# Kernel tuning notes

Hardware: AMD Instinct MI355X
Metric: run time of the kernel (lower is better)

Reference implementation:

```python
import jax, jax.numpy as jnp
import numpy as np

NM = 4096; NP = 4096; EM = 65536; EP = 65536; H = 256; HEADS = 4; G = 32


def _lin(k, din, dout):
    k1, k2 = jax.random.split(k)
    return (jax.random.normal(k1, (din, dout), jnp.float32) * (1.0 / np.sqrt(din)),
            jax.random.normal(k2, (dout,), jnp.float32) * 0.01)


def setup_inputs() -> dict:
    key = jax.random.key(0)
    ks = jax.random.split(key, 32)
    inp = {}
    inp['x_mol'] = jax.random.normal(ks[0], (NM, 8), jnp.float32)
    inp['x_prot'] = jax.random.normal(ks[1], (NP, 4), jnp.float32)
    inp['ea_mol'] = jax.random.normal(ks[2], (EM, 2), jnp.float32)
    inp['ea_prot'] = jax.random.normal(ks[3], (EP, 2), jnp.float32)
    inp['ei_mol'] = jax.random.randint(ks[4], (2, EM), 0, NM)
    inp['ei_prot'] = jax.random.randint(ks[5], (2, EP), 0, NP)
    inp['batch_mol'] = jnp.sort(jax.random.randint(ks[6], (NM,), 0, G))
    inp['batch_prot'] = jnp.sort(jax.random.randint(ks[7], (NP,), 0, G))
    inp['node_lin_mol_w'], inp['node_lin_mol_b'] = _lin(ks[8], 8, H)
    inp['node_lin_prot_w'], inp['node_lin_prot_b'] = _lin(ks[9], 4, H)
    inp['edge_lin_mol_w'], inp['edge_lin_mol_b'] = _lin(ks[10], 2, H)
    inp['edge_lin_prot_w'], inp['edge_lin_prot_b'] = _lin(ks[11], 2, H)
    # two GINE conv layers per graph, each with a 2-layer MLP; stack layer dim first
    for pref, base in (('mol', 12), ('prot', 16)):
        w1 = []; b1 = []; w2 = []; b2 = []
        for l in range(2):
            w, b = _lin(ks[base + 2 * l], H, H); w1.append(w); b1.append(b)
            w, b = _lin(ks[base + 2 * l + 1], H, H); w2.append(w); b2.append(b)
        inp[pref + '_w1'] = jnp.stack(w1); inp[pref + '_b1'] = jnp.stack(b1)
        inp[pref + '_w2'] = jnp.stack(w2); inp[pref + '_b2'] = jnp.stack(b2)
    for pref, base in (('mp', 20), ('pm', 23)):
        inp[pref + '_wq'], inp[pref + '_bq'] = _lin(ks[base], H, H)
        inp[pref + '_wk'], inp[pref + '_bk'] = _lin(ks[base + 1], H, H)
        inp[pref + '_wv'], inp[pref + '_bv'] = _lin(ks[base + 2], H, H)
    inp['fc1_w'], inp['fc1_b'] = _lin(ks[26], 2 * H, H)
    inp['fc2_w'], inp['fc2_b'] = _lin(ks[27], H, 1)
    return inp


def _gine_stack(x, ei, e, w1, b1, w2, b2):
    # GINEConv (eps=0): x_i' = relu(nn(x_i + sum_j relu(x_j + e_ji))), 2 layers, shared edge emb
    src, dst = ei[0], ei[1]
    n = x.shape[0]
    for l in range(w1.shape[0]):
        msg = jax.nn.relu(x[src] + e)                      # [E, H]
        agg = jax.ops.segment_sum(msg, dst, num_segments=n)  # [N, H]
        h = x + agg
        h = jax.nn.relu(h @ w1[l] + b1[l]) @ w2[l] + b2[l]
        x = jax.nn.relu(h)
    return x


def _cross_attn(qn, kn, wq, bq, wk, bk, wv, bv):
    nq, d = qn.shape
    nk = kn.shape[0]
    hd = d // HEADS
    Q = (qn @ wq + bq).reshape(nq, HEADS, hd)
    K = (kn @ wk + bk).reshape(nk, HEADS, hd)
    V = (kn @ wv + bv).reshape(nk, HEADS, hd)
    scores = jnp.einsum('qhd,khd->hqk', Q, K) / np.float32(hd ** 0.5)
    w = jax.nn.softmax(scores, axis=-1)
    return jnp.einsum('hqk,khd->qhd', w, V).reshape(nq, d)


def _seg_mean(h, seg, n):
    s = jax.ops.segment_sum(h, seg, num_segments=n)
    c = jax.ops.segment_sum(jnp.ones((h.shape[0], 1), h.dtype), seg, num_segments=n)
    return s / jnp.maximum(c, 1.0)


def reference(x_mol, x_prot, ea_mol, ea_prot, ei_mol, ei_prot, batch_mol, batch_prot,
              node_lin_mol_w, node_lin_mol_b, node_lin_prot_w, node_lin_prot_b,
              edge_lin_mol_w, edge_lin_mol_b, edge_lin_prot_w, edge_lin_prot_b,
              mol_w1, mol_b1, mol_w2, mol_b2, prot_w1, prot_b1, prot_w2, prot_b2,
              mp_wq, mp_bq, mp_wk, mp_bk, mp_wv, mp_bv,
              pm_wq, pm_bq, pm_wk, pm_bk, pm_wv, pm_bv,
              fc1_w, fc1_b, fc2_w, fc2_b):
    hm = x_mol @ node_lin_mol_w + node_lin_mol_b
    hp = x_prot @ node_lin_prot_w + node_lin_prot_b
    em = ea_mol @ edge_lin_mol_w + edge_lin_mol_b
    ep = ea_prot @ edge_lin_prot_w + edge_lin_prot_b
    H_mol = _gine_stack(hm, ei_mol, em, mol_w1, mol_b1, mol_w2, mol_b2)
    H_prot = _gine_stack(hp, ei_prot, ep, prot_w1, prot_b1, prot_w2, prot_b2)
    H_mol_c = H_mol + _cross_attn(H_mol, H_prot, mp_wq, mp_bq, mp_wk, mp_bk, mp_wv, mp_bv)
    H_prot_c = H_prot + _cross_attn(H_prot, H_mol, pm_wq, pm_bq, pm_wk, pm_bk, pm_wv, pm_bv)
    z_mol = _seg_mean(H_mol_c, batch_mol, G)
    z_prot = _seg_mean(H_prot_c, batch_prot, G)
    z = jnp.concatenate([z_mol, z_prot], axis=1)
    x = jax.nn.relu(z @ fc1_w + fc1_b)
    out = jax.nn.sigmoid(x @ fc2_w + fc2_b)
    return out.squeeze(-1)
```

## Files before the change

### kernel.cpp

```cpp
#include <hip/hip_runtime.h>
#include <math.h>

#define HDIM 256
#define NMOL 4096
#define NPROT 4096
#define NEDGE 65536
#define NG 32

typedef _Float16 f16x8 __attribute__((ext_vector_type(8)));
typedef _Float16 f16x4 __attribute__((ext_vector_type(4)));
typedef __attribute__((ext_vector_type(4))) float f32x4;

__device__ __forceinline__ void splitf(float x, _Float16& h, _Float16& l) {
  h = (_Float16)x;
  l = (_Float16)(x - (float)h);
}

struct __align__(16) EdgeRec { int src; float a0; float a1; int pad; };

struct PtrPack { const float* p[14]; };

__global__ __launch_bounds__(256) void k_prep_wt(PtrPack pk, _Float16* __restrict__ dh,
                                                 _Float16* __restrict__ dl) {
  __shared__ float Ts[64][68];
  const int m = blockIdx.z;
  const int n0 = blockIdx.y * 64, k0 = blockIdx.x * 64;
  const float* W = pk.p[m];
  const int t = threadIdx.x;
#pragma unroll
  for (int rep = 0; rep < 16; ++rep) {
    int k = rep * 4 + (t >> 6);
    int n = t & 63;
    Ts[n][k] = W[(size_t)(k0 + k) * 256 + n0 + n];
  }
  __syncthreads();
#pragma unroll
  for (int rep = 0; rep < 2; ++rep) {
    int idx = t + rep * 256;
    int nr = idx >> 3, koff = (idx & 7) * 8;
    f16x8 vh, vl;
#pragma unroll
    for (int i = 0; i < 8; ++i) {
      _Float16 h, l;
      splitf(Ts[nr][koff + i], h, l);
      vh[i] = h; vl[i] = l;
    }
    size_t off = (size_t)m * 65536 + (size_t)(n0 + nr) * 256 + k0 + koff;
    *(f16x8*)&dh[off] = vh;
    *(f16x8*)&dl[off] = vl;
  }
}

struct EmbJob {
  const float* x; const float* w; const float* b;
  _Float16* oh; _Float16* ol; int K;
};

__global__ __launch_bounds__(256) void k_node_embed2(EmbJob j0, EmbJob j1) {
  const EmbJob& j = blockIdx.y ? j1 : j0;
  const int i = blockIdx.x;
  const int c = threadIdx.x;
  float acc = j.b[c];
  for (int k = 0; k < j.K; ++k) acc += j.x[i * j.K + k] * j.w[k * HDIM + c];
  _Float16 h, l;
  splitf(acc, h, l);
  j.oh[(size_t)i * HDIM + c] = h;
  j.ol[(size_t)i * HDIM + c] = l;
}

__global__ __launch_bounds__(256) void k_csr_count2(const int* __restrict__ ei0,
                                                    const int* __restrict__ ei1,
                                                    int* __restrict__ cur0,
                                                    int* __restrict__ cur1, int E) {
  const int* ei = blockIdx.y ? ei1 : ei0;
  int* cur = blockIdx.y ? cur1 : cur0;
  const int e = blockIdx.x * 256 + threadIdx.x;
  if (e < E) atomicAdd(&cur[ei[E + e]], 1);
}

__global__ __launch_bounds__(256) void k_csr_scan2(int* __restrict__ c0, int* __restrict__ o0,
                                                   int* __restrict__ c1, int* __restrict__ o1,
                                                   int N) {
  int* cnt_cur = blockIdx.x ? c1 : c0;
  int* off = blockIdx.x ? o1 : o0;
  __shared__ int tsum[256], tpre[257];
  const int t = threadIdx.x;
  const int base = t * 16;
  int loc[16], s = 0;
#pragma unroll
  for (int i = 0; i < 16; ++i) { loc[i] = cnt_cur[base + i]; s += loc[i]; }
  tsum[t] = s;
  __syncthreads();
  if (t == 0) {
    int a = 0;
    for (int i = 0; i < 256; ++i) { tpre[i] = a; a += tsum[i]; }
    tpre[256] = a;
  }
  __syncthreads();
  int a = tpre[t];
#pragma unroll
  for (int i = 0; i < 16; ++i) {
    off[base + i] = a;
    cnt_cur[base + i] = a;
    a += loc[i];
  }
  if (t == 255) off[N] = tpre[256];
}

__global__ __launch_bounds__(256) void k_csr_scatter2(
    const int* __restrict__ ei0, const int* __restrict__ ei1,
    const float* __restrict__ ea0, const float* __restrict__ ea1,
    int* __restrict__ cur0, int* __restrict__ cur1,
    EdgeRec* __restrict__ er0, EdgeRec* __restrict__ er1, int E) {
  const int* ei = blockIdx.y ? ei1 : ei0;
  const float* ea = blockIdx.y ? ea1 : ea0;
  int* cur = blockIdx.y ? cur1 : cur0;
  EdgeRec* er = blockIdx.y ? er1 : er0;
  const int e = blockIdx.x * 256 + threadIdx.x;
  if (e < E) {
    int pos = atomicAdd(&cur[ei[E + e]], 1);
    EdgeRec r;
    r.src = ei[e];
    r.a0 = ea[2 * e];
    r.a1 = ea[2 * e + 1];
    r.pad = 0;
    er[pos] = r;
  }
}

struct AggJob {
  const _Float16* xh; const _Float16* xl; const EdgeRec* er;
  const int* off; const float* we; const float* be;
  _Float16* sh; _Float16* sl;
};

__global__ __launch_bounds__(256) void k_agg2(AggJob a0, AggJob a1) {
  const AggJob& a = blockIdx.y ? a1 : a0;
  const int n = blockIdx.x;
  const int c = threadIdx.x;
  const float w0 = a.we[c], w1 = a.we[HDIM + c], bb = a.be[c];
  const int j0 = a.off[n], j1 = a.off[n + 1];
  float sum = 0.f;
  int j = j0;
  for (; j + 1 < j1; j += 2) {
    EdgeRec ra = a.er[j];
    EdgeRec rb = a.er[j + 1];
    float xa = (float)a.xh[(size_t)ra.src * HDIM + c] + (float)a.xl[(size_t)ra.src * HDIM + c];
    float xb = (float)a.xh[(size_t)rb.src * HDIM + c] + (float)a.xl[(size_t)rb.src * HDIM + c];
    sum += fmaxf(xa + ra.a0 * w0 + ra.a1 * w1 + bb, 0.f);
    sum += fmaxf(xb + rb.a0 * w0 + rb.a1 * w1 + bb, 0.f);
  }
  if (j < j1) {
    EdgeRec ra = a.er[j];
    float xa = (float)a.xh[(size_t)ra.src * HDIM + c] + (float)a.xl[(size_t)ra.src * HDIM + c];
    sum += fmaxf(xa + ra.a0 * w0 + ra.a1 * w1 + bb, 0.f);
  }
  float self = (float)a.xh[(size_t)n * HDIM + c] + (float)a.xl[(size_t)n * HDIM + c];
  _Float16 h, l;
  splitf(self + sum, h, l);
  a.sh[(size_t)n * HDIM + c] = h;
  a.sl[(size_t)n * HDIM + c] = l;
}

struct GJob {
  const _Float16* Ah; const _Float16* Al;
  const _Float16* Bh; const _Float16* Bl;
  const float* bias;
  _Float16* Ch; _Float16* Cl; _Float16* Vt;
  float oscale; int flags;
};
struct GJobs { GJob j[6]; };

__global__ __launch_bounds__(256) void k_gemm(GJobs js) {
  const GJob J = js.j[blockIdx.z];
  const int relu = J.flags & 1;
  const int outmode = J.flags >> 4;
  __shared__ _Float16 Ah[64][72], Al[64][72], Bh[64][72], Bl[64][72];
  const int t = threadIdx.x;
  const int bm = blockIdx.x * 64, bn = blockIdx.y * 64;
  const int lane = t & 63, w = t >> 6;
  const int l15 = lane & 15, l4 = lane >> 4;
  const int wm = (w >> 1) * 32, wn = (w & 1) * 32;
  f32x4 acc[2][2] = {};
  for (int k0 = 0; k0 < 256; k0 += 64) {
    __syncthreads();
#pragma unroll
    for (int rep = 0; rep < 2; ++rep) {
      int idx = t + rep * 256;
      int r = idx >> 3, k8 = (idx & 7) * 8;
      size_t offa = (size_t)(bm + r) * 256 + k0 + k8;
      *(f16x8*)&Ah[r][k8] = *(const f16x8*)&J.Ah[offa];
      *(f16x8*)&Al[r][k8] = *(const f16x8*)&J.Al[offa];
      size_t offb = (size_t)(bn + r) * 256 + k0 + k8;
      *(f16x8*)&Bh[r][k8] = *(const f16x8*)&J.Bh[offb];
      *(f16x8*)&Bl[r][k8] = *(const f16x8*)&J.Bl[offb];
    }
    __syncthreads();
#pragma unroll
    for (int kh = 0; kh < 2; ++kh) {
      f16x8 a0h = *(f16x8*)&Ah[wm + l15][kh * 32 + l4 * 8];
      f16x8 a0l = *(f16x8*)&Al[wm + l15][kh * 32 + l4 * 8];
      f16x8 a1h = *(f16x8*)&Ah[wm + 16 + l15][kh * 32 + l4 * 8];
      f16x8 a1l = *(f16x8*)&Al[wm + 16 + l15][kh * 32 + l4 * 8];
      f16x8 b0h = *(f16x8*)&Bh[wn + l15][kh * 32 + l4 * 8];
      f16x8 b0l = *(f16x8*)&Bl[wn + l15][kh * 32 + l4 * 8];
      f16x8 b1h = *(f16x8*)&Bh[wn + 16 + l15][kh * 32 + l4 * 8];
      f16x8 b1l = *(f16x8*)&Bl[wn + 16 + l15][kh * 32 + l4 * 8];
      acc[0][0] = __builtin_amdgcn_mfma_f32_16x16x32_f16(a0h, b0h, acc[0][0], 0, 0, 0);
      acc[0][0] = __builtin_amdgcn_mfma_f32_16x16x32_f16(a0h, b0l, acc[0][0], 0, 0, 0);
      acc[0][0] = __builtin_amdgcn_mfma_f32_16x16x32_f16(a0l, b0h, acc[0][0], 0, 0, 0);
      acc[0][1] = __builtin_amdgcn_mfma_f32_16x16x32_f16(a0h, b1h, acc[0][1], 0, 0, 0);
      acc[0][1] = __builtin_amdgcn_mfma_f32_16x16x32_f16(a0h, b1l, acc[0][1], 0, 0, 0);
      acc[0][1] = __builtin_amdgcn_mfma_f32_16x16x32_f16(a0l, b1h, acc[0][1], 0, 0, 0);
      acc[1][0] = __builtin_amdgcn_mfma_f32_16x16x32_f16(a1h, b0h, acc[1][0], 0, 0, 0);
      acc[1][0] = __builtin_amdgcn_mfma_f32_16x16x32_f16(a1h, b0l, acc[1][0], 0, 0, 0);
      acc[1][0] = __builtin_amdgcn_mfma_f32_16x16x32_f16(a1l, b0h, acc[1][0], 0, 0, 0);
      acc[1][1] = __builtin_amdgcn_mfma_f32_16x16x32_f16(a1h, b1h, acc[1][1], 0, 0, 0);
      acc[1][1] = __builtin_amdgcn_mfma_f32_16x16x32_f16(a1h, b1l, acc[1][1], 0, 0, 0);
      acc[1][1] = __builtin_amdgcn_mfma_f32_16x16x32_f16(a1l, b1h, acc[1][1], 0, 0, 0);
    }
  }
  if (outmode == 3) __syncthreads();
#pragma unroll
  for (int mi = 0; mi < 2; ++mi)
#pragma unroll
    for (int ni = 0; ni < 2; ++ni) {
      int col = bn + wn + ni * 16 + l15;
      float bv = J.bias[col];
#pragma unroll
      for (int r = 0; r < 4; ++r) {
        int row = bm + wm + mi * 16 + l4 * 4 + r;
        float v = acc[mi][ni][r] + bv;
        if (relu) v = fmaxf(v, 0.f);
        if (outmode == 1) {
          float vs = v * J.oscale;
          _Float16 hh, ll;
          splitf(vs, hh, ll);
          J.Ch[(size_t)row * 256 + col] = hh;
          J.Cl[(size_t)row * 256 + col] = ll;
        } else {
          Ah[wn + ni * 16 + l15][wm + mi * 16 + l4 * 4 + r] = (_Float16)v;
        }
      }
    }
  if (outmode == 3) {
    __syncthreads();
#pragma unroll
    for (int rep = 0; rep < 2; ++rep) {
      int idx = t + rep * 256;
      int d = idx >> 3, n8 = (idx & 7) * 8;
      *(f16x8*)&J.Vt[(size_t)(bn + d) * 4096 + bm + n8] = *(f16x8*)&Ah[d][n8];
    }
  }
}

struct AttnArgs {
  const _Float16* Qh[2]; const _Float16* Ql[2];
  const _Float16* Kh[2]; const _Float16* Kl[2];
  const _Float16* Vth[2];
  float* Opart; float* mpart; float* lpart;
};

__global__ __launch_bounds__(256) void k_attn5(AttnArgs A, int nk_half) {
  __shared__ _Float16 Ksh[64][72], Ksl[64][72];
  __shared__ _Float16 Vsh[64][72];
  __shared__ _Float16 Psh[4][32][72];
  const int t = threadIdx.x;
  const int dir = blockIdx.y >> 2, h = blockIdx.y & 3;
  const int q0 = blockIdx.x * 128;
  const int half = blockIdx.z;
  const int kbase = half * nk_half;
  const int lane = t & 63, w = t >> 6;
  const int l15 = lane & 15, l4 = lane >> 4;
  const int qw = q0 + w * 32;

  const _Float16* Qh_g = A.Qh[dir];
  const _Float16* Ql_g = A.Ql[dir];
  const _Float16* Kh_g = A.Kh[dir];
  const _Float16* Kl_g = A.Kl[dir];
  const _Float16* Vth_g = A.Vth[dir];

  f16x8 qh[2][2], ql[2][2];
#pragma unroll
  for (int qf = 0; qf < 2; ++qf) {
    size_t qoff = (size_t)(qw + qf * 16 + l15) * 256 + h * 64;
#pragma unroll
    for (int kh = 0; kh < 2; ++kh) {
      qh[qf][kh] = *(const f16x8*)&Qh_g[qoff + kh * 32 + l4 * 8];
      ql[qf][kh] = *(const f16x8*)&Ql_g[qoff + kh * 32 + l4 * 8];
    }
  }
  f32x4 o[2][4] = {};
  float mrun[2] = {-1e30f, -1e30f};
  float lrun[2] = {0.f, 0.f};

  for (int kt = 0; kt < nk_half; kt += 64) {
    const int k0 = kbase + kt;
    __syncthreads();
#pragma unroll
    for (int rep = 0; rep < 2; ++rep) {
      int idx = t + rep * 256;
      int r = idx >> 3, c8 = idx & 7;
      size_t koff = (size_t)(k0 + r) * 256 + h * 64 + c8 * 8;
      *(f16x8*)&Ksh[r][c8 * 8] = *(const f16x8*)&Kh_g[koff];
      *(f16x8*)&Ksl[r][c8 * 8] = *(const f16x8*)&Kl_g[koff];
      int sc = c8 ^ ((r >> 3) & 7);
      size_t voff = (size_t)(h * 64 + r) * 4096 + k0 + c8 * 8;
      *(f16x8*)&Vsh[r][sc * 8] = *(const f16x8*)&Vth_g[voff];
    }
    __syncthreads();

    f32x4 sf[2][4] = {};
#pragma unroll
    for (int kc = 0; kc < 4; ++kc) {
      f16x8 kf0h = *(f16x8*)&Ksh[kc * 16 + l15][l4 * 8];
      f16x8 kf0l = *(f16x8*)&Ksl[kc * 16 + l15][l4 * 8];
      f16x8 kf1h = *(f16x8*)&Ksh[kc * 16 + l15][32 + l4 * 8];
      f16x8 kf1l = *(f16x8*)&Ksl[kc * 16 + l15][32 + l4 * 8];
#pragma unroll
      for (int qf = 0; qf < 2; ++qf) {
        sf[qf][kc] = __builtin_amdgcn_mfma_f32_16x16x32_f16(kf0h, qh[qf][0], sf[qf][kc], 0, 0, 0);
        sf[qf][kc] = __builtin_amdgcn_mfma_f32_16x16x32_f16(kf0h, ql[qf][0], sf[qf][kc], 0, 0, 0);
        sf[qf][kc] = __builtin_amdgcn_mfma_f32_16x16x32_f16(kf0l, qh[qf][0], sf[qf][kc], 0, 0, 0);
        sf[qf][kc] = __builtin_amdgcn_mfma_f32_16x16x32_f16(kf1h, qh[qf][1], sf[qf][kc], 0, 0, 0);
        sf[qf][kc] = __builtin_amdgcn_mfma_f32_16x16x32_f16(kf1h, ql[qf][1], sf[qf][kc], 0, 0, 0);
        sf[qf][kc] = __builtin_amdgcn_mfma_f32_16x16x32_f16(kf1l, qh[qf][1], sf[qf][kc], 0, 0, 0);
      }
    }

#pragma unroll
    for (int qf = 0; qf < 2; ++qf) {
      float mt = -1e30f;
#pragma unroll
      for (int kc = 0; kc < 4; ++kc) {
        float a = fmaxf(fmaxf(sf[qf][kc][0], sf[qf][kc][1]),
                        fmaxf(sf[qf][kc][2], sf[qf][kc][3]));
        mt = fmaxf(mt, a);
      }
      mt = fmaxf(mt, __shfl_xor(mt, 16, 64));
      mt = fmaxf(mt, __shfl_xor(mt, 32, 64));
      float mn = fmaxf(mrun[qf], mt);
      float alpha = __expf(mrun[qf] - mn);
      mrun[qf] = mn;
      float rs = 0.f;
#pragma unroll
      for (int kc = 0; kc < 4; ++kc) {
        float p0 = __expf(sf[qf][kc][0] - mn);
        float p1 = __expf(sf[qf][kc][1] - mn);
        float p2 = __expf(sf[qf][kc][2] - mn);
        float p3 = __expf(sf[qf][kc][3] - mn);
        rs += (p0 + p1) + (p2 + p3);
        f16x4 pv = {(_Float16)p0, (_Float16)p1, (_Float16)p2, (_Float16)p3};
        *(f16x4*)&Psh[w][qf * 16 + l15][kc * 16 + 4 * l4] = pv;
      }
      rs += __shfl_xor(rs, 16, 64);
      rs += __shfl_xor(rs, 32, 64);
      lrun[qf] = lrun[qf] * alpha + rs;
#pragma unroll
      for (int r = 0; r < 4; ++r) {
        float ar = __shfl(alpha, 4 * l4 + r, 64);
        o[qf][0][r] *= ar; o[qf][1][r] *= ar;
        o[qf][2][r] *= ar; o[qf][3][r] *= ar;
      }
    }

#pragma unroll
    for (int kh = 0; kh < 2; ++kh) {
      f16x8 pa0 = *(f16x8*)&Psh[w][l15][kh * 32 + l4 * 8];
      f16x8 pa1 = *(f16x8*)&Psh[w][16 + l15][kh * 32 + l4 * 8];
#pragma unroll
      for (int oc = 0; oc < 4; ++oc) {
        int d = oc * 16 + l15;
        int chunk = (kh * 4 + l4) ^ ((d >> 3) & 7);
        f16x8 vb = *(f16x8*)&Vsh[d][chunk * 8];
        o[0][oc] = __builtin_amdgcn_mfma_f32_16x16x32_f16(pa0, vb, o[0][oc], 0, 0, 0);
        o[1][oc] = __builtin_amdgcn_mfma_f32_16x16x32_f16(pa1, vb, o[1][oc], 0, 0, 0);
      }
    }
  }

  const int slot = dir * 2 + half;
#pragma unroll
  for (int qf = 0; qf < 2; ++qf)
#pragma unroll
    for (int oc = 0; oc < 4; ++oc) {
      int col = h * 64 + oc * 16 + l15;
#pragma unroll
      for (int r = 0; r < 4; ++r) {
        int row = qw + qf * 16 + 4 * l4 + r;
        A.Opart[((size_t)slot * 4096 + row) * 256 + col] = o[qf][oc][r];
      }
    }
  if (lane < 16) {
#pragma unroll
    for (int qf = 0; qf < 2; ++qf) {
      int row = qw + qf * 16 + l15;
      A.mpart[(size_t)(slot * 4 + h) * 4096 + row] = mrun[qf];
      A.lpart[(size_t)(slot * 4 + h) * 4096 + row] = lrun[qf];
    }
  }
}

__global__ __launch_bounds__(256) void k_combine_pool(
    const float* __restrict__ Opart, const float* __restrict__ mpart,
    const float* __restrict__ lpart,
    const _Float16* __restrict__ hmh, const _Float16* __restrict__ hml,
    const _Float16* __restrict__ hph, const _Float16* __restrict__ hpl,
    const int* __restrict__ b_mol, const int* __restrict__ b_prot,
    float* __restrict__ z, float* __restrict__ cnt) {
  const int row = blockIdx.x;
  const int dir = blockIdx.y;
  const int c = threadIdx.x;
  const int h = c >> 6;
  const _Float16* Hh = dir ? hph : hmh;
  const _Float16* Hl = dir ? hpl : hml;
  const int g = (dir ? b_prot : b_mol)[row];
  size_t mi0 = (size_t)((dir * 2 + 0) * 4 + h) * 4096 + row;
  size_t mi1 = (size_t)((dir * 2 + 1) * 4 + h) * 4096 + row;
  float m1 = mpart[mi0], m2 = mpart[mi1];
  float l1 = lpart[mi0], l2 = lpart[mi1];
  float M = fmaxf(m1, m2);
  float e1 = __expf(m1 - M), e2 = __expf(m2 - M);
  float L = l1 * e1 + l2 * e2;
  float O1 = Opart[((size_t)(dir * 2 + 0) * 4096 + row) * 256 + c];
  float O2 = Opart[((size_t)(dir * 2 + 1) * 4096 + row) * 256 + c];
  float hin = (float)Hh[(size_t)row * 256 + c] + (float)Hl[(size_t)row * 256 + c];
  float v = (O1 * e1 + O2 * e2) / L + hin;
  atomicAdd(&z[(size_t)g * 512 + dir * 256 + c], v);
  if (c == 0) atomicAdd(&cnt[dir * 32 + g], 1.0f);
}

__global__ __launch_bounds__(256) void k_head(
    const float* __restrict__ z, const float* __restrict__ cnt,
    const float* __restrict__ w1, const float* __restrict__ b1,
    const float* __restrict__ w2, const float* __restrict__ b2,
    float* __restrict__ out) {
  __shared__ float wsum[4];
  const int r = blockIdx.x;
  const int c = threadIdx.x;
  const float im = 1.0f / fmaxf(cnt[r], 1.0f);
  const float ip = 1.0f / fmaxf(cnt[32 + r], 1.0f);
  float acc = b1[c];
  for (int k = 0; k < 256; ++k) acc += (z[r * 512 + k] * im) * w1[k * HDIM + c];
  for (int k = 256; k < 512; ++k) acc += (z[r * 512 + k] * ip) * w1[k * HDIM + c];
  acc = fmaxf(acc, 0.f);
  float p = acc * w2[c];
#pragma unroll
  for (int off = 1; off < 64; off <<= 1) p += __shfl_xor(p, off, 64);
  if ((c & 63) == 0) wsum[c >> 6] = p;
  __syncthreads();
  if (c == 0) {
    float s = (wsum[0] + wsum[1]) + (wsum[2] + wsum[3]) + b2[0];
    out[r] = 1.0f / (1.0f + __expf(-s));
  }
}

extern "C" void kernel_launch(void* const* d_in, const int* in_sizes, int n_in,
                              void* d_out, int out_size, void* d_ws, size_t ws_size,
                              hipStream_t stream) {
  const float* x_mol   = (const float*)d_in[0];
  const float* x_prot  = (const float*)d_in[1];
  const float* ea_mol  = (const float*)d_in[2];
  const float* ea_prot = (const float*)d_in[3];
  const int*   ei_mol  = (const int*)d_in[4];
  const int*   ei_prot = (const int*)d_in[5];
  const int*   b_mol   = (const int*)d_in[6];
  const int*   b_prot  = (const int*)d_in[7];
  const float* nlm_w = (const float*)d_in[8];
  const float* nlm_b = (const float*)d_in[9];
  const float* nlp_w = (const float*)d_in[10];
  const float* nlp_b = (const float*)d_in[11];
  const float* elm_w = (const float*)d_in[12];
  const float* elm_b = (const float*)d_in[13];
  const float* elp_w = (const float*)d_in[14];
  const float* elp_b = (const float*)d_in[15];
  const float* mol_w1 = (const float*)d_in[16];
  const float* mol_b1 = (const float*)d_in[17];
  const float* mol_w2 = (const float*)d_in[18];
  const float* mol_b2 = (const float*)d_in[19];
  const float* prot_w1 = (const float*)d_in[20];
  const float* prot_b1 = (const float*)d_in[21];
  const float* prot_w2 = (const float*)d_in[22];
  const float* prot_b2 = (const float*)d_in[23];
  const float* mp_wq = (const float*)d_in[24];
  const float* mp_bq = (const float*)d_in[25];
  const float* mp_wk = (const float*)d_in[26];
  const float* mp_bk = (const float*)d_in[27];
  const float* mp_wv = (const float*)d_in[28];
  const float* mp_bv = (const float*)d_in[29];
  const float* pm_wq = (const float*)d_in[30];
  const float* pm_bq = (const float*)d_in[31];
  const float* pm_wk = (const float*)d_in[32];
  const float* pm_bk = (const float*)d_in[33];
  const float* pm_wv = (const float*)d_in[34];
  const float* pm_bv = (const float*)d_in[35];
  const float* fc1_w = (const float*)d_in[36];
  const float* fc1_b = (const float*)d_in[37];
  const float* fc2_w = (const float*)d_in[38];
  const float* fc2_b = (const float*)d_in[39];
  float* out = (float*)d_out;

  char* W8 = (char*)d_ws;
  const size_t MB = 1u << 20;
  _Float16* wtH  = (_Float16*)(W8 + 0 * MB);
  _Float16* wtL  = (_Float16*)(W8 + 2 * MB);
  _Float16* hmh  = (_Float16*)(W8 + 4 * MB);
  _Float16* hml  = (_Float16*)(W8 + 6 * MB);
  _Float16* hph  = (_Float16*)(W8 + 8 * MB);
  _Float16* hpl  = (_Float16*)(W8 + 10 * MB);
  _Float16* amh  = (_Float16*)(W8 + 12 * MB);
  _Float16* aml  = (_Float16*)(W8 + 14 * MB);
  _Float16* aph  = (_Float16*)(W8 + 16 * MB);
  _Float16* apl  = (_Float16*)(W8 + 18 * MB);
  _Float16* t1mh = (_Float16*)(W8 + 20 * MB);
  _Float16* t1ml = (_Float16*)(W8 + 22 * MB);
  _Float16* t1ph = (_Float16*)(W8 + 24 * MB);
  _Float16* t1pl = (_Float16*)(W8 + 26 * MB);
  _Float16* Qh0  = (_Float16*)(W8 + 28 * MB);
  _Float16* Ql0  = (_Float16*)(W8 + 30 * MB);
  _Float16* Kh0  = (_Float16*)(W8 + 32 * MB);
  _Float16* Kl0  = (_Float16*)(W8 + 34 * MB);
  _Float16* Qh1  = (_Float16*)(W8 + 36 * MB);
  _Float16* Ql1  = (_Float16*)(W8 + 38 * MB);
  _Float16* Kh1  = (_Float16*)(W8 + 40 * MB);
  _Float16* Kl1  = (_Float16*)(W8 + 42 * MB);
  _Float16* Vth0 = (_Float16*)(W8 + 44 * MB);
  _Float16* Vth1 = (_Float16*)(W8 + 46 * MB);
  float* Opart = (float*)(W8 + 48 * MB);
  float* mpart = (float*)(W8 + 64 * MB);
  float* lpart = mpart + 65536;
  float* zb    = lpart + 65536;
  float* cnt   = zb + 32 * 512;
  int* off_m = (int*)(W8 + 65 * MB);
  int* cur_m = off_m + 4224;
  int* off_p = (int*)(W8 + 66 * MB);
  int* cur_p = off_p + 4224;
  EdgeRec* er_m = (EdgeRec*)(W8 + 67 * MB);
  EdgeRec* er_p = (EdgeRec*)(W8 + 68 * MB);

  PtrPack pk;
  pk.p[0] = mol_w1;           pk.p[1] = mol_w1 + 65536;
  pk.p[2] = mol_w2;           pk.p[3] = mol_w2 + 65536;
  pk.p[4] = prot_w1;          pk.p[5] = prot_w1 + 65536;
  pk.p[6] = prot_w2;          pk.p[7] = prot_w2 + 65536;
  pk.p[8] = mp_wq;  pk.p[9] = mp_wk;  pk.p[10] = mp_wv;
  pk.p[11] = pm_wq; pk.p[12] = pm_wk; pk.p[13] = pm_wv;
  k_prep_wt<<<dim3(4, 4, 14), 256, 0, stream>>>(pk, wtH, wtL);

  hipMemsetAsync(cur_m, 0, 4096 * 4, stream);
  hipMemsetAsync(cur_p, 0, 4096 * 4, stream);
  k_csr_count2<<<dim3(NEDGE / 256, 2), 256, 0, stream>>>(ei_mol, ei_prot, cur_m, cur_p, NEDGE);
  k_csr_scan2<<<2, 256, 0, stream>>>(cur_m, off_m, cur_p, off_p, NMOL);
  k_csr_scatter2<<<dim3(NEDGE / 256, 2), 256, 0, stream>>>(ei_mol, ei_prot, ea_mol, ea_prot,
                                                           cur_m, cur_p, er_m, er_p, NEDGE);

  EmbJob em = {x_mol, nlm_w, nlm_b, hmh, hml, 8};
  EmbJob ep = {x_prot, nlp_w, nlp_b, hph, hpl, 4};
  k_node_embed2<<<dim3(NMOL, 2), 256, 0, stream>>>(em, ep);

#define WTH(i) (wtH + (size_t)(i) * 65536)
#define WTL(i) (wtL + (size_t)(i) * 65536)

  AggJob am = {hmh, hml, er_m, off_m, elm_w, elm_b, amh, aml};
  AggJob ap = {hph, hpl, er_p, off_p, elp_w, elp_b, aph, apl};

  for (int l = 0; l < 2; ++l) {
    k_agg2<<<dim3(NMOL, 2), 256, 0, stream>>>(am, ap);
    GJobs g1 = {};
    g1.j[0] = {amh, aml, WTH(l), WTL(l), mol_b1 + l * 256,
               t1mh, t1ml, nullptr, 1.0f, 1 | (1 << 4)};
    g1.j[1] = {aph, apl, WTH(4 + l), WTL(4 + l), prot_b1 + l * 256,
               t1ph, t1pl, nullptr, 1.0f, 1 | (1 << 4)};
    k_gemm<<<dim3(64, 4, 2), 256, 0, stream>>>(g1);
    GJobs g2 = {};
    g2.j[0] = {t1mh, t1ml, WTH(2 + l), WTL(2 + l), mol_b2 + l * 256,
               hmh, hml, nullptr, 1.0f, 1 | (1 << 4)};
    g2.j[1] = {t1ph, t1pl, WTH(6 + l), WTL(6 + l), prot_b2 + l * 256,
               hph, hpl, nullptr, 1.0f, 1 | (1 << 4)};
    k_gemm<<<dim3(64, 4, 2), 256, 0, stream>>>(g2);
  }

  {
    GJobs q = {};
    q.j[0] = {hmh, hml, WTH(8), WTL(8), mp_bq, Qh0, Ql0, nullptr, 0.125f, 1 << 4};
    q.j[1] = {hph, hpl, WTH(9), WTL(9), mp_bk, Kh0, Kl0, nullptr, 1.0f, 1 << 4};
    q.j[2] = {hph, hpl, WTH(10), WTL(10), mp_bv, nullptr, nullptr, Vth0, 1.0f, 3 << 4};
    q.j[3] = {hph, hpl, WTH(11), WTL(11), pm_bq, Qh1, Ql1, nullptr, 0.125f, 1 << 4};
    q.j[4] = {hmh, hml, WTH(12), WTL(12), pm_bk, Kh1, Kl1, nullptr, 1.0f, 1 << 4};
    q.j[5] = {hmh, hml, WTH(13), WTL(13), pm_bv, nullptr, nullptr, Vth1, 1.0f, 3 << 4};
    k_gemm<<<dim3(64, 4, 6), 256, 0, stream>>>(q);
  }

  AttnArgs aa;
  aa.Qh[0] = Qh0; aa.Ql[0] = Ql0; aa.Kh[0] = Kh0; aa.Kl[0] = Kl0; aa.Vth[0] = Vth0;
  aa.Qh[1] = Qh1; aa.Ql[1] = Ql1; aa.Kh[1] = Kh1; aa.Kl[1] = Kl1; aa.Vth[1] = Vth1;
  aa.Opart = Opart; aa.mpart = mpart; aa.lpart = lpart;
  k_attn5<<<dim3(32, 8, 2), 256, 0, stream>>>(aa, 2048);

  hipMemsetAsync(zb, 0, (32 * 512 + 64) * 4, stream);
  k_combine_pool<<<dim3(4096, 2), 256, 0, stream>>>(Opart, mpart, lpart,
                                                    hmh, hml, hph, hpl,
                                                    b_mol, b_prot, zb, cnt);
  k_head<<<NG, 256, 0, stream>>>(zb, cnt, fc1_w, fc1_b, fc2_w, fc2_b, out);
#undef WTH
#undef WTL
}
```

Measured before the change: 501.7 us.

## Fuse CSR build, GINE MLP pair, attention split-K and pooling head kernels

Several changes at once. The three CSR kernels and two memsets become a single two-block kernel that counts, scans and scatters in shared memory. The two GINE MLP GEMMs become one fused kernel that keeps the intermediate activation in LDS. Attention is split four ways along the key dimension instead of two, and writes its partial outputs in fp16. The combine/pool and head kernels merge into one per-graph kernel that finds each segment by binary search, which removes the atomics and the zeroing memset but leaves only 32 blocks doing the pooling.

Result: slower. 619.2 us (+23.4%).

```diff
diff --git a/kernel.cpp b/kernel.cpp
--- a/kernel.cpp
+++ b/kernel.cpp
@@ -68,57 +68,56 @@
   j.ol[(size_t)i * HDIM + c] = l;
 }
 
-__global__ __launch_bounds__(256) void k_csr_count2(const int* __restrict__ ei0,
-                                                    const int* __restrict__ ei1,
-                                                    int* __restrict__ cur0,
-                                                    int* __restrict__ cur1, int E) {
-  const int* ei = blockIdx.y ? ei1 : ei0;
-  int* cur = blockIdx.y ? cur1 : cur0;
-  const int e = blockIdx.x * 256 + threadIdx.x;
-  if (e < E) atomicAdd(&cur[ei[E + e]], 1);
-}
-
-__global__ __launch_bounds__(256) void k_csr_scan2(int* __restrict__ c0, int* __restrict__ o0,
-                                                   int* __restrict__ c1, int* __restrict__ o1,
-                                                   int N) {
-  int* cnt_cur = blockIdx.x ? c1 : c0;
-  int* off = blockIdx.x ? o1 : o0;
-  __shared__ int tsum[256], tpre[257];
+__global__ __launch_bounds__(1024) void k_csr_all(
+    const int* __restrict__ ei0, const int* __restrict__ ei1,
+    const float* __restrict__ ea0, const float* __restrict__ ea1,
+    int* __restrict__ off0, int* __restrict__ off1,
+    EdgeRec* __restrict__ er0, EdgeRec* __restrict__ er1) {
+  __shared__ int lcnt[4096];
+  __shared__ int wbase[16];
+  const int dir = blockIdx.x;
+  const int* ei = dir ? ei1 : ei0;
+  const float* ea = dir ? ea1 : ea0;
+  int* off = dir ? off1 : off0;
+  EdgeRec* er = dir ? er1 : er0;
   const int t = threadIdx.x;
-  const int base = t * 16;
-  int loc[16], s = 0;
-#pragma unroll
-  for (int i = 0; i < 16; ++i) { loc[i] = cnt_cur[base + i]; s += loc[i]; }
-  tsum[t] = s;
+  const int lane = t & 63, wv = t >> 6;
+
+#pragma unroll
+  for (int i = 0; i < 4; ++i) lcnt[t + i * 1024] = 0;
+  __syncthreads();
+  for (int e = t; e < NEDGE; e += 1024) atomicAdd(&lcnt[ei[NEDGE + e]], 1);
+  __syncthreads();
+
+  int loc[4], s = 0;
+#pragma unroll
+  for (int i = 0; i < 4; ++i) { loc[i] = lcnt[t * 4 + i]; s += loc[i]; }
+  int pre = s;
+#pragma unroll
+  for (int o = 1; o < 64; o <<= 1) {
+    int v = __shfl_up(pre, o, 64);
+    if (lane >= o) pre += v;
+  }
+  if (lane == 63) wbase[wv] = pre;
   __syncthreads();
   if (t == 0) {
     int a = 0;
-    for (int i = 0; i < 256; ++i) { tpre[i] = a; a += tsum[i]; }
-    tpre[256] = a;
-  }
-  __syncthreads();
-  int a = tpre[t];
-#pragma unroll
-  for (int i = 0; i < 16; ++i) {
-    off[base + i] = a;
-    cnt_cur[base + i] = a;
+    for (int i = 0; i < 16; ++i) { int v = wbase[i]; wbase[i] = a; a += v; }
+  }
+  __syncthreads();
+  int a = wbase[wv] + pre - s;
+#pragma unroll
+  for (int i = 0; i < 4; ++i) {
+    off[t * 4 + i] = a;
+    lcnt[t * 4 + i] = a;
     a += loc[i];
   }
-  if (t == 255) off[N] = tpre[256];
-}
-
-__global__ __launch_bounds__(256) void k_csr_scatter2(
-    const int* __restrict__ ei0, const int* __restrict__ ei1,
-    const float* __restrict__ ea0, const float* __restrict__ ea1,
-    int* __restrict__ cur0, int* __restrict__ cur1,
-    EdgeRec* __restrict__ er0, EdgeRec* __restrict__ er1, int E) {
-  const int* ei = blockIdx.y ? ei1 : ei0;
-  const float* ea = blockIdx.y ? ea1 : ea0;
-  int* cur = blockIdx.y ? cur1 : cur0;
-  EdgeRec* er = blockIdx.y ? er1 : er0;
-  const int e = blockIdx.x * 256 + threadIdx.x;
-  if (e < E) {
-    int pos = atomicAdd(&cur[ei[E + e]], 1);
+  if (t == 1023) off[4096] = a;
+  __syncthreads();
+
+  for (int e = t; e < NEDGE; e += 1024) {
+    int d = ei[NEDGE + e];
+    int pos = atomicAdd(&lcnt[d], 1);
     EdgeRec r;
     r.src = ei[e];
     r.a0 = ea[2 * e];
@@ -160,6 +159,131 @@
   splitf(self + sum, h, l);
   a.sh[(size_t)n * HDIM + c] = h;
   a.sl[(size_t)n * HDIM + c] = l;
+}
+
+struct FusedJob {
+  const _Float16* Ah; const _Float16* Al;
+  const _Float16* W1h; const _Float16* W1l; const float* b1;
+  const _Float16* W2h; const _Float16* W2l; const float* b2;
+  _Float16* Oh; _Float16* Ol;
+};
+
+__global__ __launch_bounds__(256) void k_gine_fused(FusedJob j0, FusedJob j1) {
+  const FusedJob J = blockIdx.y ? j1 : j0;
+  __shared__ _Float16 Bh[4][64][72], Bl[4][64][72];
+  __shared__ _Float16 Ast_h[4][32][72], Ast_l[4][32][72];
+  const int t = threadIdx.x;
+  const int bm = blockIdx.x * 32;
+  const int lane = t & 63, w = t >> 6;
+  const int l15 = lane & 15, l4 = lane >> 4;
+
+#pragma unroll
+  for (int rep = 0; rep < 4; ++rep) {
+    int idx = t + rep * 256;
+    int r = idx >> 5;
+    int c8 = idx & 31;
+    size_t off = (size_t)(bm + r) * 256 + c8 * 8;
+    *(f16x8*)&Ast_h[c8 >> 3][r][(c8 & 7) * 8] = *(const f16x8*)&J.Ah[off];
+    *(f16x8*)&Ast_l[c8 >> 3][r][(c8 & 7) * 8] = *(const f16x8*)&J.Al[off];
+  }
+  __syncthreads();
+
+  f32x4 acc[2][4] = {};
+  for (int k0 = 0; k0 < 4; ++k0) {
+#pragma unroll
+    for (int rep = 0; rep < 8; ++rep) {
+      int idx = lane + rep * 64;
+      int nr = idx >> 3, c8 = idx & 7;
+      size_t off = (size_t)(w * 64 + nr) * 256 + k0 * 64 + c8 * 8;
+      *(f16x8*)&Bh[w][nr][c8 * 8] = *(const f16x8*)&J.W1h[off];
+      *(f16x8*)&Bl[w][nr][c8 * 8] = *(const f16x8*)&J.W1l[off];
+    }
+#pragma unroll
+    for (int kh = 0; kh < 2; ++kh) {
+      f16x8 a0h = *(f16x8*)&Ast_h[k0][l15][kh * 32 + l4 * 8];
+      f16x8 a0l = *(f16x8*)&Ast_l[k0][l15][kh * 32 + l4 * 8];
+      f16x8 a1h = *(f16x8*)&Ast_h[k0][16 + l15][kh * 32 + l4 * 8];
+      f16x8 a1l = *(f16x8*)&Ast_l[k0][16 + l15][kh * 32 + l4 * 8];
+#pragma unroll
+      for (int ni = 0; ni < 4; ++ni) {
+        f16x8 bh = *(f16x8*)&Bh[w][ni * 16 + l15][kh * 32 + l4 * 8];
+        f16x8 bl = *(f16x8*)&Bl[w][ni * 16 + l15][kh * 32 + l4 * 8];
+        acc[0][ni] = __builtin_amdgcn_mfma_f32_16x16x32_f16(a0h, bh, acc[0][ni], 0, 0, 0);
+        acc[0][ni] = __builtin_amdgcn_mfma_f32_16x16x32_f16(a0h, bl, acc[0][ni], 0, 0, 0);
+        acc[0][ni] = __builtin_amdgcn_mfma_f32_16x16x32_f16(a0l, bh, acc[0][ni], 0, 0, 0);
+        acc[1][ni] = __builtin_amdgcn_mfma_f32_16x16x32_f16(a1h, bh, acc[1][ni], 0, 0, 0);
+        acc[1][ni] = __builtin_amdgcn_mfma_f32_16x16x32_f16(a1h, bl, acc[1][ni], 0, 0, 0);
+        acc[1][ni] = __builtin_amdgcn_mfma_f32_16x16x32_f16(a1l, bh, acc[1][ni], 0, 0, 0);
+      }
+    }
+  }
+  __syncthreads();
+#pragma unroll
+  for (int mi = 0; mi < 2; ++mi)
+#pragma unroll
+    for (int ni = 0; ni < 4; ++ni) {
+      int cl = ni * 16 + l15;
+      float bv = J.b1[w * 64 + cl];
+#pragma unroll
+      for (int r = 0; r < 4; ++r) {
+        int row = mi * 16 + l4 * 4 + r;
+        float v = fmaxf(acc[mi][ni][r] + bv, 0.f);
+        _Float16 hh, ll;
+        splitf(v, hh, ll);
+        Ast_h[w][row][cl] = hh;
+        Ast_l[w][row][cl] = ll;
+      }
+    }
+  __syncthreads();
+
+#pragma unroll
+  for (int mi = 0; mi < 2; ++mi)
+#pragma unroll
+    for (int ni = 0; ni < 4; ++ni) acc[mi][ni] = (f32x4){0.f, 0.f, 0.f, 0.f};
+  for (int k0 = 0; k0 < 4; ++k0) {
+#pragma unroll
+    for (int rep = 0; rep < 8; ++rep) {
+      int idx = lane + rep * 64;
+      int nr = idx >> 3, c8 = idx & 7;
+      size_t off = (size_t)(w * 64 + nr) * 256 + k0 * 64 + c8 * 8;
+      *(f16x8*)&Bh[w][nr][c8 * 8] = *(const f16x8*)&J.W2h[off];
+      *(f16x8*)&Bl[w][nr][c8 * 8] = *(const f16x8*)&J.W2l[off];
+    }
+#pragma unroll
+    for (int kh = 0; kh < 2; ++kh) {
+      f16x8 a0h = *(f16x8*)&Ast_h[k0][l15][kh * 32 + l4 * 8];
+      f16x8 a0l = *(f16x8*)&Ast_l[k0][l15][kh * 32 + l4 * 8];
+      f16x8 a1h = *(f16x8*)&Ast_h[k0][16 + l15][kh * 32 + l4 * 8];
+      f16x8 a1l = *(f16x8*)&Ast_l[k0][16 + l15][kh * 32 + l4 * 8];
+#pragma unroll
+      for (int ni = 0; ni < 4; ++ni) {
+        f16x8 bh = *(f16x8*)&Bh[w][ni * 16 + l15][kh * 32 + l4 * 8];
+        f16x8 bl = *(f16x8*)&Bl[w][ni * 16 + l15][kh * 32 + l4 * 8];
+        acc[0][ni] = __builtin_amdgcn_mfma_f32_16x16x32_f16(a0h, bh, acc[0][ni], 0, 0, 0);
+        acc[0][ni] = __builtin_amdgcn_mfma_f32_16x16x32_f16(a0h, bl, acc[0][ni], 0, 0, 0);
+        acc[0][ni] = __builtin_amdgcn_mfma_f32_16x16x32_f16(a0l, bh, acc[0][ni], 0, 0, 0);
+        acc[1][ni] = __builtin_amdgcn_mfma_f32_16x16x32_f16(a1h, bh, acc[1][ni], 0, 0, 0);
+        acc[1][ni] = __builtin_amdgcn_mfma_f32_16x16x32_f16(a1h, bl, acc[1][ni], 0, 0, 0);
+        acc[1][ni] = __builtin_amdgcn_mfma_f32_16x16x32_f16(a1l, bh, acc[1][ni], 0, 0, 0);
+      }
+    }
+  }
+#pragma unroll
+  for (int mi = 0; mi < 2; ++mi)
+#pragma unroll
+    for (int ni = 0; ni < 4; ++ni) {
+      int col = w * 64 + ni * 16 + l15;
+      float bv = J.b2[col];
+#pragma unroll
+      for (int r = 0; r < 4; ++r) {
+        int row = bm + mi * 16 + l4 * 4 + r;
+        float v = fmaxf(acc[mi][ni][r] + bv, 0.f);
+        _Float16 hh, ll;
+        splitf(v, hh, ll);
+        J.Oh[(size_t)row * 256 + col] = hh;
+        J.Ol[(size_t)row * 256 + col] = ll;
+      }
+    }
 }
 
 struct GJob {
@@ -258,18 +382,18 @@
   const _Float16* Qh[2]; const _Float16* Ql[2];
   const _Float16* Kh[2]; const _Float16* Kl[2];
   const _Float16* Vth[2];
-  float* Opart; float* mpart; float* lpart;
+  _Float16* Opart; float* mpart; float* lpart;
 };
 
-__global__ __launch_bounds__(256) void k_attn5(AttnArgs A, int nk_half) {
+__global__ __launch_bounds__(256) void k_attn6(AttnArgs A, int nkq) {
   __shared__ _Float16 Ksh[64][72], Ksl[64][72];
   __shared__ _Float16 Vsh[64][72];
   __shared__ _Float16 Psh[4][32][72];
   const int t = threadIdx.x;
   const int dir = blockIdx.y >> 2, h = blockIdx.y & 3;
   const int q0 = blockIdx.x * 128;
-  const int half = blockIdx.z;
-  const int kbase = half * nk_half;
+  const int quarter = blockIdx.z;
+  const int kbase = quarter * nkq;
   const int lane = t & 63, w = t >> 6;
   const int l15 = lane & 15, l4 = lane >> 4;
   const int qw = q0 + w * 32;
@@ -294,7 +418,7 @@
   float mrun[2] = {-1e30f, -1e30f};
   float lrun[2] = {0.f, 0.f};
 
-  for (int kt = 0; kt < nk_half; kt += 64) {
+  for (int kt = 0; kt < nkq; kt += 64) {
     const int k0 = kbase + kt;
     __syncthreads();
 #pragma unroll
@@ -379,7 +503,7 @@
     }
   }
 
-  const int slot = dir * 2 + half;
+  const int slot = dir * 4 + quarter;
 #pragma unroll
   for (int qf = 0; qf < 2; ++qf)
 #pragma unroll
@@ -388,7 +512,7 @@
 #pragma unroll
       for (int r = 0; r < 4; ++r) {
         int row = qw + qf * 16 + 4 * l4 + r;
-        A.Opart[((size_t)slot * 4096 + row) * 256 + col] = o[qf][oc][r];
+        A.Opart[((size_t)slot * 4096 + row) * 256 + col] = (_Float16)o[qf][oc][r];
       }
     }
   if (lane < 16) {
@@ -401,48 +525,55 @@
   }
 }
 
-__global__ __launch_bounds__(256) void k_combine_pool(
-    const float* __restrict__ Opart, const float* __restrict__ mpart,
+__global__ __launch_bounds__(256) void k_head_all(
+    const _Float16* __restrict__ Opart, const float* __restrict__ mpart,
     const float* __restrict__ lpart,
     const _Float16* __restrict__ hmh, const _Float16* __restrict__ hml,
     const _Float16* __restrict__ hph, const _Float16* __restrict__ hpl,
     const int* __restrict__ b_mol, const int* __restrict__ b_prot,
-    float* __restrict__ z, float* __restrict__ cnt) {
-  const int row = blockIdx.x;
-  const int dir = blockIdx.y;
-  const int c = threadIdx.x;
-  const int h = c >> 6;
-  const _Float16* Hh = dir ? hph : hmh;
-  const _Float16* Hl = dir ? hpl : hml;
-  const int g = (dir ? b_prot : b_mol)[row];
-  size_t mi0 = (size_t)((dir * 2 + 0) * 4 + h) * 4096 + row;
-  size_t mi1 = (size_t)((dir * 2 + 1) * 4 + h) * 4096 + row;
-  float m1 = mpart[mi0], m2 = mpart[mi1];
-  float l1 = lpart[mi0], l2 = lpart[mi1];
-  float M = fmaxf(m1, m2);
-  float e1 = __expf(m1 - M), e2 = __expf(m2 - M);
-  float L = l1 * e1 + l2 * e2;
-  float O1 = Opart[((size_t)(dir * 2 + 0) * 4096 + row) * 256 + c];
-  float O2 = Opart[((size_t)(dir * 2 + 1) * 4096 + row) * 256 + c];
-  float hin = (float)Hh[(size_t)row * 256 + c] + (float)Hl[(size_t)row * 256 + c];
-  float v = (O1 * e1 + O2 * e2) / L + hin;
-  atomicAdd(&z[(size_t)g * 512 + dir * 256 + c], v);
-  if (c == 0) atomicAdd(&cnt[dir * 32 + g], 1.0f);
-}
-
-__global__ __launch_bounds__(256) void k_head(
-    const float* __restrict__ z, const float* __restrict__ cnt,
     const float* __restrict__ w1, const float* __restrict__ b1,
     const float* __restrict__ w2, const float* __restrict__ b2,
     float* __restrict__ out) {
+  __shared__ float zl[512];
   __shared__ float wsum[4];
-  const int r = blockIdx.x;
+  const int g = blockIdx.x;
   const int c = threadIdx.x;
-  const float im = 1.0f / fmaxf(cnt[r], 1.0f);
-  const float ip = 1.0f / fmaxf(cnt[32 + r], 1.0f);
+  const int h = c >> 6;
+  for (int dir = 0; dir < 2; ++dir) {
+    const int* batch = dir ? b_prot : b_mol;
+    const _Float16* Hh = dir ? hph : hmh;
+    const _Float16* Hl = dir ? hpl : hml;
+    int lo = 0, hi = 4096;
+    while (lo < hi) { int mid = (lo + hi) >> 1; if (batch[mid] < g) lo = mid + 1; else hi = mid; }
+    int start = lo;
+    lo = 0; hi = 4096;
+    while (lo < hi) { int mid = (lo + hi) >> 1; if (batch[mid] < g + 1) lo = mid + 1; else hi = mid; }
+    int end = lo;
+    float zacc = 0.f;
+    for (int row = start; row < end; ++row) {
+      float mv[4], lv[4], M = -1e30f;
+#pragma unroll
+      for (int q = 0; q < 4; ++q) {
+        int slot = dir * 4 + q;
+        mv[q] = mpart[(size_t)(slot * 4 + h) * 4096 + row];
+        lv[q] = lpart[(size_t)(slot * 4 + h) * 4096 + row];
+        M = fmaxf(M, mv[q]);
+      }
+      float L = 0.f, acc = 0.f;
+#pragma unroll
+      for (int q = 0; q < 4; ++q) {
+        float e = __expf(mv[q] - M);
+        L += lv[q] * e;
+        acc += (float)Opart[((size_t)(dir * 4 + q) * 4096 + row) * 256 + c] * e;
+      }
+      float hin = (float)Hh[(size_t)row * 256 + c] + (float)Hl[(size_t)row * 256 + c];
+      zacc += acc / L + hin;
+    }
+    zl[dir * 256 + c] = zacc / fmaxf((float)(end - start), 1.0f);
+  }
+  __syncthreads();
   float acc = b1[c];
-  for (int k = 0; k < 256; ++k) acc += (z[r * 512 + k] * im) * w1[k * HDIM + c];
-  for (int k = 256; k < 512; ++k) acc += (z[r * 512 + k] * ip) * w1[k * HDIM + c];
+  for (int k = 0; k < 512; ++k) acc += zl[k] * w1[k * HDIM + c];
   acc = fmaxf(acc, 0.f);
   float p = acc * w2[c];
 #pragma unroll
@@ -451,7 +582,7 @@
   __syncthreads();
   if (c == 0) {
     float s = (wsum[0] + wsum[1]) + (wsum[2] + wsum[3]) + b2[0];
-    out[r] = 1.0f / (1.0f + __expf(-s));
+    out[g] = 1.0f / (1.0f + __expf(-s));
   }
 }
 
@@ -512,31 +643,23 @@
   _Float16* aml  = (_Float16*)(W8 + 14 * MB);
   _Float16* aph  = (_Float16*)(W8 + 16 * MB);
   _Float16* apl  = (_Float16*)(W8 + 18 * MB);
-  _Float16* t1mh = (_Float16*)(W8 + 20 * MB);
-  _Float16* t1ml = (_Float16*)(W8 + 22 * MB);
-  _Float16* t1ph = (_Float16*)(W8 + 24 * MB);
-  _Float16* t1pl = (_Float16*)(W8 + 26 * MB);
-  _Float16* Qh0  = (_Float16*)(W8 + 28 * MB);
-  _Float16* Ql0  = (_Float16*)(W8 + 30 * MB);
-  _Float16* Kh0  = (_Float16*)(W8 + 32 * MB);
-  _Float16* Kl0  = (_Float16*)(W8 + 34 * MB);
-  _Float16* Qh1  = (_Float16*)(W8 + 36 * MB);
-  _Float16* Ql1  = (_Float16*)(W8 + 38 * MB);
-  _Float16* Kh1  = (_Float16*)(W8 + 40 * MB);
-  _Float16* Kl1  = (_Float16*)(W8 + 42 * MB);
-  _Float16* Vth0 = (_Float16*)(W8 + 44 * MB);
-  _Float16* Vth1 = (_Float16*)(W8 + 46 * MB);
-  float* Opart = (float*)(W8 + 48 * MB);
-  float* mpart = (float*)(W8 + 64 * MB);
-  float* lpart = mpart + 65536;
-  float* zb    = lpart + 65536;
-  float* cnt   = zb + 32 * 512;
-  int* off_m = (int*)(W8 + 65 * MB);
-  int* cur_m = off_m + 4224;
-  int* off_p = (int*)(W8 + 66 * MB);
-  int* cur_p = off_p + 4224;
-  EdgeRec* er_m = (EdgeRec*)(W8 + 67 * MB);
-  EdgeRec* er_p = (EdgeRec*)(W8 + 68 * MB);
+  _Float16* Qh0  = (_Float16*)(W8 + 20 * MB);
+  _Float16* Ql0  = (_Float16*)(W8 + 22 * MB);
+  _Float16* Kh0  = (_Float16*)(W8 + 24 * MB);
+  _Float16* Kl0  = (_Float16*)(W8 + 26 * MB);
+  _Float16* Qh1  = (_Float16*)(W8 + 28 * MB);
+  _Float16* Ql1  = (_Float16*)(W8 + 30 * MB);
+  _Float16* Kh1  = (_Float16*)(W8 + 32 * MB);
+  _Float16* Kl1  = (_Float16*)(W8 + 34 * MB);
+  _Float16* Vth0 = (_Float16*)(W8 + 36 * MB);
+  _Float16* Vth1 = (_Float16*)(W8 + 38 * MB);
+  _Float16* Opart = (_Float16*)(W8 + 40 * MB);
+  float* mpart = (float*)(W8 + 56 * MB);
+  float* lpart = (float*)(W8 + 56 * MB + 512 * 1024);
+  int* off_m = (int*)(W8 + 57 * MB);
+  int* off_p = off_m + 8192;
+  EdgeRec* er_m = (EdgeRec*)(W8 + 58 * MB);
+  EdgeRec* er_p = (EdgeRec*)(W8 + 59 * MB);
 
   PtrPack pk;
   pk.p[0] = mol_w1;           pk.p[1] = mol_w1 + 65536;
@@ -547,12 +670,8 @@
   pk.p[11] = pm_wq; pk.p[12] = pm_wk; pk.p[13] = pm_wv;
   k_prep_wt<<<dim3(4, 4, 14), 256, 0, stream>>>(pk, wtH, wtL);
 
-  hipMemsetAsync(cur_m, 0, 4096 * 4, stream);
-  hipMemsetAsync(cur_p, 0, 4096 * 4, stream);
-  k_csr_count2<<<dim3(NEDGE / 256, 2), 256, 0, stream>>>(ei_mol, ei_prot, cur_m, cur_p, NEDGE);
-  k_csr_scan2<<<2, 256, 0, stream>>>(cur_m, off_m, cur_p, off_p, NMOL);
-  k_csr_scatter2<<<dim3(NEDGE / 256, 2), 256, 0, stream>>>(ei_mol, ei_prot, ea_mol, ea_prot,
-                                                           cur_m, cur_p, er_m, er_p, NEDGE);
+  k_csr_all<<<2, 1024, 0, stream>>>(ei_mol, ei_prot, ea_mol, ea_prot,
+                                    off_m, off_p, er_m, er_p);
 
   EmbJob em = {x_mol, nlm_w, nlm_b, hmh, hml, 8};
   EmbJob ep = {x_prot, nlp_w, nlp_b, hph, hpl, 4};
@@ -566,18 +685,11 @@
 
   for (int l = 0; l < 2; ++l) {
     k_agg2<<<dim3(NMOL, 2), 256, 0, stream>>>(am, ap);
-    GJobs g1 = {};
-    g1.j[0] = {amh, aml, WTH(l), WTL(l), mol_b1 + l * 256,
-               t1mh, t1ml, nullptr, 1.0f, 1 | (1 << 4)};
-    g1.j[1] = {aph, apl, WTH(4 + l), WTL(4 + l), prot_b1 + l * 256,
-               t1ph, t1pl, nullptr, 1.0f, 1 | (1 << 4)};
-    k_gemm<<<dim3(64, 4, 2), 256, 0, stream>>>(g1);
-    GJobs g2 = {};
-    g2.j[0] = {t1mh, t1ml, WTH(2 + l), WTL(2 + l), mol_b2 + l * 256,
-               hmh, hml, nullptr, 1.0f, 1 | (1 << 4)};
-    g2.j[1] = {t1ph, t1pl, WTH(6 + l), WTL(6 + l), prot_b2 + l * 256,
-               hph, hpl, nullptr, 1.0f, 1 | (1 << 4)};
-    k_gemm<<<dim3(64, 4, 2), 256, 0, stream>>>(g2);
+    FusedJob fm = {amh, aml, WTH(l), WTL(l), mol_b1 + l * 256,
+                   WTH(2 + l), WTL(2 + l), mol_b2 + l * 256, hmh, hml};
+    FusedJob fp = {aph, apl, WTH(4 + l), WTL(4 + l), prot_b1 + l * 256,
+                   WTH(6 + l), WTL(6 + l), prot_b2 + l * 256, hph, hpl};
+    k_gine_fused<<<dim3(128, 2), 256, 0, stream>>>(fm, fp);
   }
 
   {
@@ -595,13 +707,10 @@
   aa.Qh[0] = Qh0; aa.Ql[0] = Ql0; aa.Kh[0] = Kh0; aa.Kl[0] = Kl0; aa.Vth[0] = Vth0;
   aa.Qh[1] = Qh1; aa.Ql[1] = Ql1; aa.Kh[1] = Kh1; aa.Kl[1] = Kl1; aa.Vth[1] = Vth1;
   aa.Opart = Opart; aa.mpart = mpart; aa.lpart = lpart;
-  k_attn5<<<dim3(32, 8, 2), 256, 0, stream>>>(aa, 2048);
-
-  hipMemsetAsync(zb, 0, (32 * 512 + 64) * 4, stream);
-  k_combine_pool<<<dim3(4096, 2), 256, 0, stream>>>(Opart, mpart, lpart,
-                                                    hmh, hml, hph, hpl,
-                                                    b_mol, b_prot, zb, cnt);
-  k_head<<<NG, 256, 0, stream>>>(zb, cnt, fc1_w, fc1_b, fc2_w, fc2_b, out);
+  k_attn6<<<dim3(32, 8, 4), 256, 0, stream>>>(aa, 1024);
+
+  k_head_all<<<NG, 256, 0, stream>>>(Opart, mpart, lpart, hmh, hml, hph, hpl,
+                                     b_mol, b_prot, fc1_w, fc1_b, fc2_w, fc2_b, out);
 #undef WTH
 #undef WTL
 }
```
